# Performance work log

Measured on AMD Instinct MI355X. Metric: run time of the kernel, lower is better.

Reference implementation:

```python
import jax, jax.numpy as jnp
import numpy as np

B, P, K, L = 16, 1024, 20, 10  # clouds, points/cloud, knn k, cov rank l
NCLS = 40


def _jacobi3(A, iters=5):
    """Batched 3x3 symmetric eigendecomposition via cyclic Jacobi sweeps.
    Returns (eigvals (N,3), V (N,3,3)) with ROWS of V as eigenvectors,
    mimicking diag(cov, nr_iterations=5)."""
    N = A.shape[0]
    V = jnp.broadcast_to(jnp.eye(3, dtype=A.dtype), (N, 3, 3))
    for _ in range(iters):
        for (p, q) in ((0, 1), (0, 2), (1, 2)):
            app, aqq, apq = A[:, p, p], A[:, q, q], A[:, p, q]
            nz = jnp.abs(apq) > 1e-12
            denom = jnp.where(nz, 2.0 * apq, 1.0)
            tau = (aqq - app) / denom
            t = jnp.where(nz, jnp.sign(tau) / (jnp.abs(tau) + jnp.sqrt(1.0 + tau * tau)), 0.0)
            c = 1.0 / jnp.sqrt(1.0 + t * t)
            s = t * c
            G = jnp.broadcast_to(jnp.eye(3, dtype=A.dtype), (N, 3, 3))
            G = G.at[:, p, p].set(c).at[:, q, q].set(c).at[:, p, q].set(s).at[:, q, p].set(-s)
            A = jnp.einsum('nia,nik,nkb->nab', G, A, G)  # G^T A G
            V = jnp.einsum('nik,nkb->nib', V, G)          # V @ G (columns = eigvecs)
    S = jnp.diagonal(A, axis1=1, axis2=2)
    return S, jnp.swapaxes(V, 1, 2)  # rows = eigenvectors


def _knn_edges(pos):
    """k-NN within each cloud (no self loops). Returns (center, nbr) global idx, grouped per center."""
    pb = pos.reshape(B, P, 3)
    sq = jnp.sum(pb * pb, axis=-1)                             # (B,P)
    d2 = sq[:, :, None] + sq[:, None, :] - 2.0 * jnp.einsum('bpc,bqc->bpq', pb, pb)
    d2 = d2 + jnp.eye(P, dtype=pos.dtype)[None] * 1e10         # mask self
    _, idx = jax.lax.top_k(-d2, K)                             # (B,P,K) nearest
    offs = (jnp.arange(B, dtype=idx.dtype) * P)[:, None, None]
    nbr = (idx + offs).reshape(-1)                             # (B*P*K,)
    center = jnp.repeat(jnp.arange(B * P, dtype=idx.dtype), K)
    return center, nbr


def setup_inputs() -> dict:
    key = jax.random.key(0)
    ks = jax.random.split(key, 14)
    def lin(k, fi, fo):
        return jax.random.normal(k, (fi, fo), jnp.float32) / np.sqrt(fi)
    inp = {
        'pos': jax.random.normal(ks[0], (B * P, 3), jnp.float32),
        'W1': lin(ks[1], 3, 32),   'b1': jnp.zeros((32,), jnp.float32),
        'W2': lin(ks[2], 32, 15),  'b2': jnp.zeros((15,), jnp.float32),
        'W3': lin(ks[3], 18, 256), 'b3': jnp.zeros((256,), jnp.float32),
        'W4': lin(ks[4], 256, 256),'b4': jnp.zeros((256,), jnp.float32),
        'Wn1': lin(ks[5], 256, 256), 'bn1': jnp.zeros((256,), jnp.float32),
        'Wn2': lin(ks[6], 256, NCLS), 'bn2': jnp.zeros((NCLS,), jnp.float32),
        'batch': jnp.repeat(jnp.arange(B, dtype=jnp.int64), P),
    }
    return inp


def reference(pos, W1, b1, W2, b2, W3, b3, W4, b4, Wn1, bn1, Wn2, bn2, batch):
    N = B * P
    center, nbr = _knn_edges(pos)
    # per-point neighbor clusters (gather): (N, K, 3)
    clusters = pos[nbr].reshape(N, K, 3) - pos[:, None, :]
    # local covariance from first L neighbors + iterative eigendecomposition
    cov = jnp.einsum('nki,nkj->nij', clusters[:, :L], clusters[:, :L])
    _, V = _jacobi3(cov, iters=5)
    # reorient clusters: bmm(clusters, V^T)
    dir_clusters = jnp.einsum('nkj,nij->nki', clusters, V)
    signs = jnp.sign(jnp.sum(dir_clusters[:, :, 2], axis=1))
    dir_clusters = jnp.concatenate(
        [dir_clusters[:, :, :2], (dir_clusters[:, :, 2] * signs[:, None])[:, :, None]], axis=2)
    # DirectionalSplineConv3D (proxy): per-edge MLP on reoriented offsets, sum over k -> (N,15)
    h = jax.nn.relu(dir_clusters @ W1 + b1)
    feat = jax.nn.sigmoid(jnp.sum(h @ W2 + b2, axis=1))  # sigmoid as in SampleNetDD
    # DirectionalDense: gather neighbor features, rotate 3-groups, concat, per-edge MLP, sum
    cf = feat[nbr].reshape(N, K * 5, 3)                   # (E,15) -> (N, 5K, 3)
    dir_feat = jnp.einsum('nmj,nij->nmi', cf, V).reshape(N, K, 15)
    concat = jnp.concatenate([dir_clusters, dir_feat], axis=2)  # (N,K,18)
    h2 = jax.nn.relu(concat @ W3 + b3)
    h2 = jax.nn.relu(h2 @ W4 + b4)
    point_feat = jnp.sum(h2, axis=1)                      # (N,256)
    # mean-pool per cloud + head
    ys = point_feat.reshape(B, P, 256).mean(axis=1)
    y1 = jax.nn.elu(ys @ Wn1 + bn1)
    y2 = jax.nn.log_softmax(y1 @ Wn2 + bn2, axis=1)
    return y2
```

## Files before the change

kernel.cpp:

```cpp
#include <hip/hip_runtime.h>
#include <hip/hip_bf16.h>
#include <math.h>

#define NB   16
#define NP   1024
#define KN   20
#define LN   10
#define NPT  16384
#define NCLS 40

typedef short bf16x8 __attribute__((ext_vector_type(8)));
typedef float f32x4  __attribute__((ext_vector_type(4)));
typedef unsigned long long u64;

__device__ __forceinline__ short f2bf(float x) {
    __hip_bfloat16 h = __float2bfloat16(x);
    return *reinterpret_cast<short*>(&h);
}
__device__ __forceinline__ float bf2f(short s) {
    unsigned u = ((unsigned)(unsigned short)s) << 16;
    return __uint_as_float(u);
}
__device__ __forceinline__ unsigned pack2bf(float lo, float hi) {
    return (unsigned)(unsigned short)f2bf(lo) | ((unsigned)(unsigned short)f2bf(hi) << 16);
}

__global__ __launch_bounds__(256) void prep_k(const float* __restrict__ W3,
                                              const float* __restrict__ W4,
                                              short* __restrict__ W3T,
                                              short* __restrict__ W4T)
{
    const int k = blockIdx.x;
    const int n = threadIdx.x;
    W4T[n * 256 + k] = f2bf(W4[k * 256 + n]);
    if (k < 32) {
        float v = (k < 18) ? W3[k * 256 + n] : 0.0f;
        W3T[n * 32 + k] = f2bf(v);
    }
}

__global__ __launch_bounds__(256, 2) void knn_k(const float* __restrict__ pos,
                                                int* __restrict__ nbr)
{
    __shared__ float4 sp[NP];
    const int t    = threadIdx.x;
    const int blk  = blockIdx.x;
    const int b    = blk >> 6;
    const int base = b * NP;

    for (int i = t; i < NP; i += 256) {
        float x = pos[(base + i) * 3 + 0];
        float y = pos[(base + i) * 3 + 1];
        float z = pos[(base + i) * 3 + 2];
        sp[i] = make_float4(x, y, z, x * x + y * y + z * z);
    }
    __syncthreads();

    const int s    = t & 15;
    const int cLoc = (blk & 63) * 16 + (t >> 4);
    const float4 cp = sp[cLoc];

    u64 A[20];
#pragma unroll
    for (int k = 0; k < 20; ++k) A[k] = ~0ull;

    const int q0 = s * 64;
    for (int ii = 0; ii < 64; ++ii) {
        int i = (ii + s) & 63;
        int q = q0 + i;
        float4 p = sp[q];
        float dot = cp.x * p.x + cp.y * p.y + cp.z * p.z;
        float d2  = (cp.w + p.w) - 2.0f * dot;
        unsigned u = __float_as_uint(d2);
        u ^= (unsigned)(((int)u >> 31) | 0x80000000);
        u64 key = ((u64)u << 32) | (unsigned)q;
        if (q == cLoc) key = ~0ull;
        if (key < A[19]) {
            A[19] = key;
#pragma unroll
            for (int j = 19; j > 0; --j)
                if (A[j] < A[j - 1]) { u64 tmp = A[j]; A[j] = A[j - 1]; A[j - 1] = tmp; }
        }
    }

#pragma unroll
    for (int m = 1; m <= 8; m <<= 1) {
        u64 Bv[20];
#pragma unroll
        for (int k = 0; k < 20; ++k) Bv[k] = __shfl_xor(A[k], m);
        u64 L[32];
#pragma unroll
        for (int i = 0; i < 12; ++i) L[i] = A[i];
#pragma unroll
        for (int i = 12; i < 20; ++i) L[i] = (A[i] < Bv[31 - i]) ? A[i] : Bv[31 - i];
#pragma unroll
        for (int i = 20; i < 32; ++i) L[i] = Bv[31 - i];
#pragma unroll
        for (int d = 16; d >= 1; d >>= 1)
#pragma unroll
            for (int i = 0; i < 32; ++i)
                if ((i & d) == 0) {
                    u64 lo = (L[i] < L[i + d]) ? L[i] : L[i + d];
                    u64 hi = (L[i] < L[i + d]) ? L[i + d] : L[i];
                    L[i] = lo; L[i + d] = hi;
                }
#pragma unroll
        for (int k = 0; k < 20; ++k) A[k] = L[k];
    }

    if (s == 0) {
        const int n = base + cLoc;
#pragma unroll
        for (int k = 0; k < 20; ++k)
            nbr[n * KN + k] = base + (int)(unsigned)(A[k] & 0xFFFFFFFFull);
    }
}

__device__ __forceinline__ void jrot(float& app, float& aqq, float& apq,
                                     float& apr, float& aqr,
                                     float& vp0, float& vp1, float& vp2,
                                     float& vq0, float& vq1, float& vq2)
{
    bool  nz    = fabsf(apq) > 1e-12f;
    float denom = nz ? 2.0f * apq : 1.0f;
    float tau   = (aqq - app) / denom;
    float sg    = (tau > 0.0f) ? 1.0f : ((tau < 0.0f) ? -1.0f : 0.0f);
    float t     = nz ? sg / (fabsf(tau) + sqrtf(1.0f + tau * tau)) : 0.0f;
    float c     = 1.0f / sqrtf(1.0f + t * t);
    float s     = t * c;

    float app_n = c * c * app - 2.0f * c * s * apq + s * s * aqq;
    float aqq_n = s * s * app + 2.0f * c * s * apq + c * c * aqq;
    float apq_n = c * s * (app - aqq) + (c * c - s * s) * apq;
    float apr_n = c * apr - s * aqr;
    float aqr_n = s * apr + c * aqr;
    app = app_n; aqq = aqq_n; apq = apq_n; apr = apr_n; aqr = aqr_n;

    float t0;
    t0 = c * vp0 - s * vq0; vq0 = s * vp0 + c * vq0; vp0 = t0;
    t0 = c * vp1 - s * vq1; vq1 = s * vp1 + c * vq1; vp1 = t0;
    t0 = c * vp2 - s * vq2; vq2 = s * vp2 + c * vq2; vp2 = t0;
}

__global__ __launch_bounds__(64) void geom_k(const float* __restrict__ pos,
                                             const int* __restrict__ nbr,
                                             const float* __restrict__ W1,
                                             const float* __restrict__ b1,
                                             const float* __restrict__ W2,
                                             const float* __restrict__ b2,
                                             float* __restrict__ dirc,
                                             short* __restrict__ featO,
                                             float* __restrict__ Vg)
{
    __shared__ float sW1[96], sb1[32], sb2[15], sW2[480];
    const int tid = threadIdx.x;
    for (int i = tid; i < 96;  i += 64) sW1[i] = W1[i];
    if (tid < 32) sb1[tid] = b1[tid];
    for (int i = tid; i < 480; i += 64) sW2[i] = W2[i];
    if (tid < 15) sb2[tid] = b2[tid];
    __syncthreads();

    const int n = blockIdx.x * 64 + tid;
    const float px = pos[n * 3 + 0], py = pos[n * 3 + 1], pz = pos[n * 3 + 2];

    float cl[KN][3];
#pragma unroll
    for (int k = 0; k < KN; ++k) {
        int j = nbr[n * KN + k];
        cl[k][0] = pos[j * 3 + 0] - px;
        cl[k][1] = pos[j * 3 + 1] - py;
        cl[k][2] = pos[j * 3 + 2] - pz;
    }

    float a00 = 0, a01 = 0, a02 = 0, a11 = 0, a12 = 0, a22 = 0;
#pragma unroll
    for (int k = 0; k < LN; ++k) {
        a00 += cl[k][0] * cl[k][0]; a01 += cl[k][0] * cl[k][1]; a02 += cl[k][0] * cl[k][2];
        a11 += cl[k][1] * cl[k][1]; a12 += cl[k][1] * cl[k][2]; a22 += cl[k][2] * cl[k][2];
    }

    float v00 = 1, v01 = 0, v02 = 0,
          v10 = 0, v11 = 1, v12 = 0,
          v20 = 0, v21 = 0, v22 = 1;
#pragma unroll
    for (int it = 0; it < 5; ++it) {
        jrot(a00, a11, a01, a02, a12, v00, v10, v20, v01, v11, v21);
        jrot(a00, a22, a02, a01, a12, v00, v10, v20, v02, v12, v22);
        jrot(a11, a22, a12, a01, a02, v01, v11, v21, v02, v12, v22);
    }

    float s2 = 0.0f;
#pragma unroll
    for (int k = 0; k < KN; ++k) {
        float d0 = cl[k][0] * v00 + cl[k][1] * v10 + cl[k][2] * v20;
        float d1 = cl[k][0] * v01 + cl[k][1] * v11 + cl[k][2] * v21;
        float d2 = cl[k][0] * v02 + cl[k][1] * v12 + cl[k][2] * v22;
        cl[k][0] = d0; cl[k][1] = d1; cl[k][2] = d2;
        s2 += d2;
    }
    float sg = (s2 > 0.0f) ? 1.0f : ((s2 < 0.0f) ? -1.0f : 0.0f);

#pragma unroll
    for (int k = 0; k < KN; ++k) {
        cl[k][2] *= sg;
        dirc[n * 60 + k * 3 + 0] = cl[k][0];
        dirc[n * 60 + k * 3 + 1] = cl[k][1];
        dirc[n * 60 + k * 3 + 2] = cl[k][2];
    }

    float hs[32];
#pragma unroll
    for (int c = 0; c < 32; ++c) {
        float w0 = sW1[c], w1 = sW1[32 + c], w2 = sW1[64 + c], bb = sb1[c];
        float acc = 0.0f;
#pragma unroll
        for (int k = 0; k < KN; ++k)
            acc += fmaxf(bb + cl[k][0] * w0 + cl[k][1] * w1 + cl[k][2] * w2, 0.0f);
        hs[c] = acc;
    }

    Vg[n * 9 + 0] = v00; Vg[n * 9 + 1] = v10; Vg[n * 9 + 2] = v20;
    Vg[n * 9 + 3] = v01; Vg[n * 9 + 4] = v11; Vg[n * 9 + 5] = v21;
    Vg[n * 9 + 6] = v02; Vg[n * 9 + 7] = v12; Vg[n * 9 + 8] = v22;

#pragma unroll
    for (int j = 0; j < 15; ++j) {
        float x = 20.0f * sb2[j];
#pragma unroll
        for (int c = 0; c < 32; ++c) x += hs[c] * sW2[c * 15 + j];
        featO[n * 15 + j] = f2bf(1.0f / (1.0f + expf(-x)));
    }
}

__global__ __launch_bounds__(256, 4) void mlp_k(const int* __restrict__ nbr,
                                                const float* __restrict__ dirc,
                                                const short* __restrict__ featB,
                                                const float* __restrict__ Vg,
                                                const short* __restrict__ W3T,
                                                const float* __restrict__ b3,
                                                const short* __restrict__ W4T,
                                                const float* __restrict__ b4,
                                                float* __restrict__ pf)
{
    __shared__ __align__(16) short H1L[64 * 256];
    __shared__ __align__(16) short concatL[64 * 40];
    __shared__ short sfeatS[60 * 16];
    __shared__ int   nbr_s[60];
    __shared__ float Vr_s[27];

    const int t   = threadIdx.x;
    const int l   = t & 63;
    const int lg  = l >> 4;
    const int lc  = l & 15;
    const int n0w = (t >> 6) * 64;
    const int pt0 = blockIdx.x * 3;
    const int swz = (lc & 7) << 3;

    if (t < 60) {
        int pt = pt0 + t / 20;
        nbr_s[t] = (pt < NPT) ? nbr[pt * 20 + (t % 20)] : 0;
    }
    if (t >= 64 && t < 91) {
        int e = t - 64;
        int pt = pt0 + e / 9;
        Vr_s[e] = (pt < NPT) ? Vg[pt * 9 + (e % 9)] : 0.0f;
    }
    for (int i = t; i < 1280; i += 256) ((int*)concatL)[i] = 0;
    __syncthreads();

    for (int i2 = t; i2 < 900; i2 += 256) {
        int nb = i2 / 15, c = i2 - nb * 15;
        sfeatS[nb * 16 + c] = featB[nbr_s[nb] * 15 + c];
    }
    __syncthreads();

    for (int job = t; job < 1080; job += 256) {
        int p  = job / 360;
        int rr = job - p * 360;
        int k  = rr / 18;
        int c  = rr - k * 18;
        int pt = pt0 + p;
        float val = 0.0f;
        if (pt < NPT) {
            if (c < 3) {
                val = dirc[pt * 60 + k * 3 + c];
            } else {
                int e = c - 3, g = e / 3, i = e - g * 3;
                const short* fr = &sfeatS[(p * 20 + k) * 16 + g * 3];
                const float* Vr = Vr_s + p * 9;
                val = bf2f(fr[0]) * Vr[i * 3 + 0] + bf2f(fr[1]) * Vr[i * 3 + 1] + bf2f(fr[2]) * Vr[i * 3 + 2];
            }
        }
        concatL[(p * 20 + k) * 40 + c] = f2bf(val);
    }
    __syncthreads();

    {
        f32x4 accB[4][4];
#pragma unroll
        for (int mt = 0; mt < 4; ++mt)
#pragma unroll
            for (int nt = 0; nt < 4; ++nt)
#pragma unroll
                for (int r = 0; r < 4; ++r) accB[mt][nt][r] = 0.0f;

        bf16x8 aB[4], bB[4];
#pragma unroll
        for (int nt = 0; nt < 4; ++nt)
            aB[nt] = *(const bf16x8*)&concatL[(nt * 16 + lc) * 40 + lg * 8];
#pragma unroll
        for (int mt = 0; mt < 4; ++mt)
            bB[mt] = *(const bf16x8*)&W3T[(n0w + mt * 16 + lc) * 32 + lg * 8];
#pragma unroll
        for (int mt = 0; mt < 4; ++mt)
#pragma unroll
            for (int nt = 0; nt < 4; ++nt)
                accB[mt][nt] = __builtin_amdgcn_mfma_f32_16x16x32_bf16(bB[mt], aB[nt], accB[mt][nt], 0, 0, 0);

#pragma unroll
        for (int mt = 0; mt < 4; ++mt) {
            const int dim0 = n0w + mt * 16 + lg * 4;
            const float4 b3q = *(const float4*)&b3[dim0];
#pragma unroll
            for (int nt = 0; nt < 4; ++nt) {
                const int row = nt * 16 + lc;
                uint2 w;
                w.x = pack2bf(fmaxf(accB[mt][nt][0] + b3q.x, 0.0f),
                              fmaxf(accB[mt][nt][1] + b3q.y, 0.0f));
                w.y = pack2bf(fmaxf(accB[mt][nt][2] + b3q.z, 0.0f),
                              fmaxf(accB[mt][nt][3] + b3q.w, 0.0f));
                *reinterpret_cast<uint2*>(&H1L[row * 256 + (dim0 ^ swz)]) = w;
            }
        }
    }
    __syncthreads();

    f32x4 acc[4][4];
#pragma unroll
    for (int mt = 0; mt < 4; ++mt)
#pragma unroll
        for (int nt = 0; nt < 4; ++nt)
#pragma unroll
            for (int r = 0; r < 4; ++r) acc[mt][nt][r] = 0.0f;

#pragma unroll
    for (int ch = 0; ch < 8; ++ch) {
        bf16x8 a[4], b[4];
#pragma unroll
        for (int mt = 0; mt < 4; ++mt)
            a[mt] = *(const bf16x8*)&H1L[(mt * 16 + lc) * 256 + ((ch * 32 + lg * 8) ^ swz)];
#pragma unroll
        for (int nt = 0; nt < 4; ++nt)
            b[nt] = *(const bf16x8*)&W4T[(n0w + nt * 16 + lc) * 256 + ch * 32 + lg * 8];
#pragma unroll
        for (int mt = 0; mt < 4; ++mt)
#pragma unroll
            for (int nt = 0; nt < 4; ++nt)
                acc[mt][nt] = __builtin_amdgcn_mfma_f32_16x16x32_bf16(a[mt], b[nt], acc[mt][nt], 0, 0, 0);
    }

    const float m1 = (lg == 0) ? 1.0f : 0.0f;
    const float m2 = (lg <  2) ? 1.0f : 0.0f;
    const float m3 = (lg <  3) ? 1.0f : 0.0f;
    const int v0 = (pt0 + 0) < NPT, v1 = (pt0 + 1) < NPT, v2 = (pt0 + 2) < NPT;
#pragma unroll
    for (int nt = 0; nt < 4; ++nt) {
        int col = n0w + nt * 16 + lc;
        float b4v = b4[col];
        float a0 = 0.0f, a1 = 0.0f, a2 = 0.0f, a3 = 0.0f;
#pragma unroll
        for (int r = 0; r < 4; ++r) {
            a0 += fmaxf(acc[0][nt][r] + b4v, 0.0f);
            a1 += fmaxf(acc[1][nt][r] + b4v, 0.0f);
            a2 += fmaxf(acc[2][nt][r] + b4v, 0.0f);
            a3 += fmaxf(acc[3][nt][r] + b4v, 0.0f);
        }
        float s0 = a0 + m1 * a1;
        float s1 = (1.0f - m1) * a1 + m2 * a2;
        float s2 = (1.0f - m2) * a2 + m3 * a3;
        s0 += __shfl_xor(s0, 16); s0 += __shfl_xor(s0, 32);
        s1 += __shfl_xor(s1, 16); s1 += __shfl_xor(s1, 32);
        s2 += __shfl_xor(s2, 16); s2 += __shfl_xor(s2, 32);
        if (l < 16) {
            if (v0) pf[(pt0 + 0) * 256 + col] = s0;
            if (v1) pf[(pt0 + 1) * 256 + col] = s1;
            if (v2) pf[(pt0 + 2) * 256 + col] = s2;
        }
    }
}

__global__ __launch_bounds__(256) void psum_k(const float* __restrict__ pf,
                                              float* __restrict__ partial)
{
    const int t   = threadIdx.x;
    const int blk = blockIdx.x;
    const int b   = blk >> 5, sl = blk & 31;
    const float* basep = pf + ((size_t)b * NP + sl * 32) * 256 + t;
    float s = 0.0f;
#pragma unroll 8
    for (int p = 0; p < 32; ++p) s += basep[p * 256];
    partial[blk * 256 + t] = s;
}

__global__ __launch_bounds__(256) void head2_k(const float* __restrict__ partial,
                                               const float* __restrict__ Wn1,
                                               const float* __restrict__ bn1,
                                               const float* __restrict__ Wn2,
                                               const float* __restrict__ bn2,
                                               float* __restrict__ out)
{
    __shared__ float ysh[256], y1h[256], zsh[64];
    const int t = threadIdx.x, b = blockIdx.x;

    float s = 0.0f;
#pragma unroll
    for (int sl = 0; sl < 32; ++sl) s += partial[(b * 32 + sl) * 256 + t];
    ysh[t] = s * (1.0f / 1024.0f);
    __syncthreads();

    float acc = bn1[t];
    for (int c = 0; c < 256; ++c) acc += ysh[c] * Wn1[c * 256 + t];
    y1h[t] = (acc > 0.0f) ? acc : expm1f(acc);
    __syncthreads();

    if (t < NCLS) {
        float z = bn2[t];
        for (int c = 0; c < 256; ++c) z += y1h[c] * Wn2[c * NCLS + t];
        zsh[t] = z;
    }
    __syncthreads();

    if (t < 64) {
        float v = (t < NCLS) ? zsh[t] : -3.0e38f;
        float m = v;
#pragma unroll
        for (int off = 32; off >= 1; off >>= 1) m = fmaxf(m, __shfl_xor(m, off));
        float e = (t < NCLS) ? expf(zsh[t] - m) : 0.0f;
#pragma unroll
        for (int off = 32; off >= 1; off >>= 1) e += __shfl_xor(e, off);
        if (t < NCLS) out[b * NCLS + t] = zsh[t] - m - logf(e);
    }
}

extern "C" void kernel_launch(void* const* d_in, const int* in_sizes, int n_in,
                              void* d_out, int out_size, void* d_ws, size_t ws_size,
                              hipStream_t stream)
{
    const float* pos = (const float*)d_in[0];
    const float* W1  = (const float*)d_in[1];
    const float* b1  = (const float*)d_in[2];
    const float* W2  = (const float*)d_in[3];
    const float* b2  = (const float*)d_in[4];
    const float* W3  = (const float*)d_in[5];
    const float* b3  = (const float*)d_in[6];
    const float* W4  = (const float*)d_in[7];
    const float* b4  = (const float*)d_in[8];
    const float* Wn1 = (const float*)d_in[9];
    const float* bn1 = (const float*)d_in[10];
    const float* Wn2 = (const float*)d_in[11];
    const float* bn2 = (const float*)d_in[12];
    float* out = (float*)d_out;

    char* ws = (char*)d_ws;
    int*   nbr     = (int*)(ws + 0);
    float* dirc    = (float*)(ws + 1310720);
    short* feat    = (short*)(ws + 5242880);
    float* Vg      = (float*)(ws + 6225920);
    float* pf      = (float*)(ws + 6815744);
    short* W4T     = (short*)(ws + 23592960);
    short* W3T     = (short*)(ws + 23724032);
    float* partial = (float*)(ws + 5242880);

    prep_k <<<256,            256, 0, stream>>>(W3, W4, W3T, W4T);
    knn_k  <<<1024,           256, 0, stream>>>(pos, nbr);
    geom_k <<<256,             64, 0, stream>>>(pos, nbr, W1, b1, W2, b2, dirc, feat, Vg);
    mlp_k  <<<(NPT + 2) / 3,  256, 0, stream>>>(nbr, dirc, feat, Vg, W3T, b3, W4T, b4, pf);
    psum_k <<<512,            256, 0, stream>>>(pf, partial);
    head2_k<<<NB,             256, 0, stream>>>(partial, Wn1, bn1, Wn2, bn2, out);
}
```

Baseline: 356.8 us.

## Fuse per-cloud pooling into MLP kernel via atomics and drop partial-sum kernel

The MLP kernel now atomically adds each point's 256-wide feature into a per-cloud sum buffer, which is zeroed by a memset, instead of writing a 16 MB per-point feature array. This removes the psum kernel and the round trip of that array through memory. It also drops the shared neighbour-index staging and one barrier by reading neighbour indices directly in the gather loop. In exchange, many blocks now contend with atomics on only 4096 addresses, and the floating-point summation order becomes nondeterministic.

```diff
diff --git a/kernel.cpp b/kernel.cpp
--- a/kernel.cpp
+++ b/kernel.cpp
@@ -240,12 +240,11 @@
                                                 const float* __restrict__ b3,
                                                 const short* __restrict__ W4T,
                                                 const float* __restrict__ b4,
-                                                float* __restrict__ pf)
+                                                float* __restrict__ ysum)
 {
     __shared__ __align__(16) short H1L[64 * 256];
     __shared__ __align__(16) short concatL[64 * 40];
     __shared__ short sfeatS[60 * 16];
-    __shared__ int   nbr_s[60];
     __shared__ float Vr_s[27];
 
     const int t   = threadIdx.x;
@@ -256,21 +255,18 @@
     const int pt0 = blockIdx.x * 3;
     const int swz = (lc & 7) << 3;
 
-    if (t < 60) {
-        int pt = pt0 + t / 20;
-        nbr_s[t] = (pt < NPT) ? nbr[pt * 20 + (t % 20)] : 0;
-    }
     if (t >= 64 && t < 91) {
         int e = t - 64;
         int pt = pt0 + e / 9;
         Vr_s[e] = (pt < NPT) ? Vg[pt * 9 + (e % 9)] : 0.0f;
     }
     for (int i = t; i < 1280; i += 256) ((int*)concatL)[i] = 0;
-    __syncthreads();
 
     for (int i2 = t; i2 < 900; i2 += 256) {
         int nb = i2 / 15, c = i2 - nb * 15;
-        sfeatS[nb * 16 + c] = featB[nbr_s[nb] * 15 + c];
+        int gi = pt0 * 20 + nb;
+        int idx = (gi < NPT * 20) ? nbr[gi] : 0;
+        sfeatS[nb * 16 + c] = featB[idx * 15 + c];
     }
     __syncthreads();
 
@@ -363,6 +359,7 @@
     const float m2 = (lg <  2) ? 1.0f : 0.0f;
     const float m3 = (lg <  3) ? 1.0f : 0.0f;
     const int v0 = (pt0 + 0) < NPT, v1 = (pt0 + 1) < NPT, v2 = (pt0 + 2) < NPT;
+    const int b0 = (pt0 + 0) >> 10, b1v = (pt0 + 1) >> 10, b2v = (pt0 + 2) >> 10;
 #pragma unroll
     for (int nt = 0; nt < 4; ++nt) {
         int col = n0w + nt * 16 + lc;
@@ -382,27 +379,14 @@
         s1 += __shfl_xor(s1, 16); s1 += __shfl_xor(s1, 32);
         s2 += __shfl_xor(s2, 16); s2 += __shfl_xor(s2, 32);
         if (l < 16) {
-            if (v0) pf[(pt0 + 0) * 256 + col] = s0;
-            if (v1) pf[(pt0 + 1) * 256 + col] = s1;
-            if (v2) pf[(pt0 + 2) * 256 + col] = s2;
+            if (v0) atomicAdd(&ysum[b0 * 256 + col], s0);
+            if (v1) atomicAdd(&ysum[b1v * 256 + col], s1);
+            if (v2) atomicAdd(&ysum[b2v * 256 + col], s2);
         }
     }
 }
 
-__global__ __launch_bounds__(256) void psum_k(const float* __restrict__ pf,
-                                              float* __restrict__ partial)
-{
-    const int t   = threadIdx.x;
-    const int blk = blockIdx.x;
-    const int b   = blk >> 5, sl = blk & 31;
-    const float* basep = pf + ((size_t)b * NP + sl * 32) * 256 + t;
-    float s = 0.0f;
-#pragma unroll 8
-    for (int p = 0; p < 32; ++p) s += basep[p * 256];
-    partial[blk * 256 + t] = s;
-}
-
-__global__ __launch_bounds__(256) void head2_k(const float* __restrict__ partial,
+__global__ __launch_bounds__(256) void head2_k(const float* __restrict__ ysum,
                                                const float* __restrict__ Wn1,
                                                const float* __restrict__ bn1,
                                                const float* __restrict__ Wn2,
@@ -412,10 +396,7 @@
     __shared__ float ysh[256], y1h[256], zsh[64];
     const int t = threadIdx.x, b = blockIdx.x;
 
-    float s = 0.0f;
-#pragma unroll
-    for (int sl = 0; sl < 32; ++sl) s += partial[(b * 32 + sl) * 256 + t];
-    ysh[t] = s * (1.0f / 1024.0f);
+    ysh[t] = ysum[b * 256 + t] * (1.0f / 1024.0f);
     __syncthreads();
 
     float acc = bn1[t];
@@ -462,19 +443,18 @@
     float* out = (float*)d_out;
 
     char* ws = (char*)d_ws;
-    int*   nbr     = (int*)(ws + 0);
-    float* dirc    = (float*)(ws + 1310720);
-    short* feat    = (short*)(ws + 5242880);
-    float* Vg      = (float*)(ws + 6225920);
-    float* pf      = (float*)(ws + 6815744);
-    short* W4T     = (short*)(ws + 23592960);
-    short* W3T     = (short*)(ws + 23724032);
-    float* partial = (float*)(ws + 5242880);
-
+    int*   nbr  = (int*)(ws + 0);
+    float* dirc = (float*)(ws + 1310720);
+    short* feat = (short*)(ws + 5242880);
+    float* Vg   = (float*)(ws + 5734400);
+    float* ysum = (float*)(ws + 6324224);
+    short* W4T  = (short*)(ws + 6340608);
+    short* W3T  = (short*)(ws + 6471680);
+
+    hipMemsetAsync(ysum, 0, NB * 256 * sizeof(float), stream);
     prep_k <<<256,            256, 0, stream>>>(W3, W4, W3T, W4T);
     knn_k  <<<1024,           256, 0, stream>>>(pos, nbr);
     geom_k <<<256,             64, 0, stream>>>(pos, nbr, W1, b1, W2, b2, dirc, feat, Vg);
-    mlp_k  <<<(NPT + 2) / 3,  256, 0, stream>>>(nbr, dirc, feat, Vg, W3T, b3, W4T, b4, pf);
-    psum_k <<<512,            256, 0, stream>>>(pf, partial);
-    head2_k<<<NB,             256, 0, stream>>>(partial, Wn1, bn1, Wn2, bn2, out);
-}
+    mlp_k  <<<(NPT + 2) / 3,  256, 0, stream>>>(nbr, dirc, feat, Vg, W3T, b3, W4T, b4, ysum);
+    head2_k<<<NB,             256, 0, stream>>>(ysum, Wn1, bn1, Wn2, bn2, out);
+}
```

Result: slower. 404.3 us (+13.3%).
